# Performance work log

Hardware: AMD Instinct MI355X
Metric: run time of the kernel (lower is better)

## Reference

```python
import jax, jax.numpy as jnp
import numpy as np

N = 31            # number of multiplexed frames; S-matrix order (2**5 - 1)
IMG_H, IMG_W = 256, 256


def make_S_mat(n):
    # Sylvester Hadamard matrix of order n+1, then standard S-matrix:
    # drop first row/col, map +1 -> 0, -1 -> 1 (binary 0/1 mask matrix).
    H = np.array([[1]], dtype=np.int64)
    while H.shape[0] < n + 1:
        H = np.block([[H, H], [H, -H]])
    return ((1 - H[1:, 1:]) * 0.5).astype(np.float32)


def setup_inputs() -> dict:
    key = jax.random.key(0)
    k1, k2 = jax.random.split(key)
    # time_points initialized near ones (Solver.initialize uses ones_like)
    time_points = jax.random.uniform(k1, (IMG_H, IMG_W, N, 1), jnp.float32, 0.5, 1.5)
    # pixels are positive photon counts
    pixels = jax.random.uniform(k2, (IMG_H, IMG_W, N, 1), jnp.float32, 1.0, 100.0)
    S = jnp.asarray(make_S_mat(N))
    t = jnp.float32(0.1)  # log-barrier weight t_init
    return {"time_points": time_points, "pixels": pixels, "S": S, "t": t}


def reference(time_points, pixels, S, t):
    # One Newton step residual: residual = J^T H^{-1} J per pixel.
    x, k = time_points, pixels            # (..., n, 1)
    n = S.shape[0]
    rate = jnp.matmul(S, x)               # (..., n, 1), assumed > 0
    inv_rate = 1.0 / rate
    inv_sq_rate = jnp.squeeze(inv_rate * inv_rate, -1)   # (..., n)

    # Jacobian: t * likelihood + time-point barrier + rate barrier
    J = (-t * jnp.matmul(S.T, k * inv_rate - 1.0)
         - 1.0 / x
         - jnp.matmul(S.T, inv_rate))     # (..., n, 1)

    # Hessian: weighted Gram S^T diag(w) S (fuses likelihood + rate-barrier
    # terms; identical math to the einsum over the SS outer-product tensor)
    w = (t * jnp.squeeze(k, -1) + 1.0) * inv_sq_rate      # (..., n)
    H = jnp.einsum('...a,da,ea->...de', w, S, S)          # (..., n, n)
    # + diag(1/x^2) time-point barrier Hessian
    H = H + (1.0 / jnp.squeeze(x * x, -1))[..., :, None] * jnp.eye(n, dtype=H.dtype)

    Hinv = jnp.linalg.inv(H)              # (..., n, n) batched inverse
    residual = jnp.squeeze(jnp.swapaxes(J, -2, -1) @ Hinv @ J, (-1, -2))  # (H, W)
    return residual
```

## Files before the change

kernel.cpp:

```cpp
#include <hip/hip_runtime.h>

#define NDIM 31
#define NPIX (256 * 256)
#define CG_FULL 3

__device__ __forceinline__ float rcpf(float x) { return __builtin_amdgcn_rcpf(x); }

template <int CTRL>
__device__ __forceinline__ float dppf(float v) {
    return __int_as_float(__builtin_amdgcn_update_dpp(
        0, __float_as_int(v), CTRL, 0xF, 0xF, true));
}
__device__ __forceinline__ float swz4(float v) {
    return __int_as_float(__builtin_amdgcn_ds_swizzle(__float_as_int(v), 0x101F));
}
__device__ __forceinline__ float swz16(float v) {
    return __int_as_float(__builtin_amdgcn_ds_swizzle(__float_as_int(v), 0x401F));
}
__device__ __forceinline__ float bperm0(float v, int bbase) {
    return __int_as_float(__builtin_amdgcn_ds_bpermute(bbase, __float_as_int(v)));
}

struct Sgn { float s1, s2, s4, s8, s16; };

__device__ __forceinline__ float wht32(float v, const Sgn& g) {
    v = fmaf(g.s1,  v, dppf<0xB1>(v));
    v = fmaf(g.s2,  v, dppf<0x4E>(v));
    v = fmaf(g.s4,  v, swz4(v));
    v = fmaf(g.s8,  v, dppf<0x128>(v));
    v = fmaf(g.s16, v, swz16(v));
    return v;
}

__device__ __forceinline__ float sum32(float s) {
    s += dppf<0xB1>(s);
    s += dppf<0x4E>(s);
    s += dppf<0x124>(s);
    s += dppf<0x128>(s);
    s += swz16(s);
    return s;
}

__global__ __launch_bounds__(256, 8) void solver_kernel(
    const float* __restrict__ xg, const float* __restrict__ kg,
    const float* __restrict__ tg, float* __restrict__ out)
{
    const int tid = blockIdx.x * 256 + threadIdx.x;
    const int pix = tid >> 5;
    const int lane = threadIdx.x & 63;
    const int l = lane & 31;
    const int bbase = (lane & 32) << 2;

    const float t = tg[0];

    float x = 1.0f, k = 0.0f;
    if (l >= 1) {
        const int base = pix * NDIM + (l - 1);
        x = xg[base];
        k = kg[base];
    }

    Sgn g;
    g.s1  = (l & 1)  ? -1.0f : 1.0f;
    g.s2  = (l & 2)  ? -1.0f : 1.0f;
    g.s4  = (l & 4)  ? -1.0f : 1.0f;
    g.s8  = (l & 8)  ? -1.0f : 1.0f;
    g.s16 = (l & 16) ? -1.0f : 1.0f;

    float xh = wht32(x, g);
    float xh0 = bperm0(xh, bbase);
    float rate = 0.5f * (xh0 - xh);
    float inv_rate = (l == 0) ? 0.0f : rcpf(rate);

    float v = t * (k * inv_rate - 1.0f) + inv_rate;
    float w = (t * k + 1.0f) * inv_rate * inv_rate;

    float invx = rcpf(x);
    float invx2 = invx * invx;

    float vh = wht32(v, g);
    float vh0 = bperm0(vh, bbase);
    float b = -0.5f * (vh0 - vh) - invx;
    if (l == 0) b = 0.0f;

    float wh = wht32(w, g);
    float wh0 = bperm0(wh, bbase);
    float dH = 0.5f * (wh0 - wh) + invx2;
    float Minv = (l == 0) ? 0.0f : rcpf(dH);

    const float w4 = 0.25f * w;

    float r = b;
    float z = Minv * r;
    float p = z;
    float rz = sum32(r * z);
    float phi = 0.0f;

#pragma unroll
    for (int it = 0; it < CG_FULL; ++it) {
        float ph = wht32(p, g);
        float ph0 = bperm0(ph, bbase);
        float q = w4 * (ph0 - ph);
        float qh = wht32(q, g);
        float qh0 = bperm0(qh, bbase);
        float Ap = fmaf(invx2, p, qh0 - qh);

        float pAp = sum32(p * Ap);
        float alpha = rz * rcpf(fmaxf(pAp, 1e-30f));
        phi = fmaf(alpha, rz, phi);
        r = fmaf(-alpha, Ap, r);
        z = Minv * r;
        float rzn = sum32(r * z);
        float beta = rzn * rcpf(fmaxf(rz, 1e-30f));
        rz = rzn;
        p = fmaf(beta, p, z);
    }
    {
        float ph = wht32(p, g);
        float ph0 = bperm0(ph, bbase);
        float q = w4 * (ph0 - ph);
        float qh = wht32(q, g);
        float qh0 = bperm0(qh, bbase);
        float Ap = fmaf(invx2, p, qh0 - qh);
        float pAp = sum32(p * Ap);
        float alpha = rz * rcpf(fmaxf(pAp, 1e-30f));
        phi = fmaf(alpha, rz, phi);
    }

    if (l == 0) out[pix] = phi;
}

extern "C" void kernel_launch(void* const* d_in, const int* in_sizes, int n_in,
                              void* d_out, int out_size, void* d_ws, size_t ws_size,
                              hipStream_t stream) {
    const float* xg = (const float*)d_in[0];
    const float* kg = (const float*)d_in[1];
    const float* tg = (const float*)d_in[3];
    float* out = (float*)d_out;

    const int threads = 256;
    const int blocks = (NPIX * 32) / threads;
    solver_kernel<<<blocks, threads, 0, stream>>>(xg, kg, tg, out);
}
```

Before: 79.12 us.

## Switch to one-thread-per-pixel with register-resident WHT and LDS-staged loads

Replaces the 32-lanes-per-pixel mapping, which used DPP and swizzle cross-lane Walsh-Hadamard transforms and reductions, with one thread per pixel. Each thread holds its 31-element vectors in registers and runs the butterfly WHT locally. Inputs are staged through shared memory with coalesced global loads, and the final CG iteration computes pAp directly from the transformed vector, skipping the second transform. The aim is to remove cross-lane shuffle and reduction latency and to cut the thread count by 32x. In exchange, register pressure becomes very high, launch bounds drop to one block, and only 256 blocks run with 62KB of LDS each, which can leave occupancy and latency hiding low.

Result: faster. 75.47 us (-4.6%).

```diff
diff --git a/kernel.cpp b/kernel.cpp
--- a/kernel.cpp
+++ b/kernel.cpp
@@ -3,131 +3,147 @@
 #define NDIM 31
 #define NPIX (256 * 256)
 #define CG_FULL 3
+#define TPB 256
+#define BLK_DW (TPB * NDIM)
 
 __device__ __forceinline__ float rcpf(float x) { return __builtin_amdgcn_rcpf(x); }
 
-template <int CTRL>
-__device__ __forceinline__ float dppf(float v) {
-    return __int_as_float(__builtin_amdgcn_update_dpp(
-        0, __float_as_int(v), CTRL, 0xF, 0xF, true));
-}
-__device__ __forceinline__ float swz4(float v) {
-    return __int_as_float(__builtin_amdgcn_ds_swizzle(__float_as_int(v), 0x101F));
-}
-__device__ __forceinline__ float swz16(float v) {
-    return __int_as_float(__builtin_amdgcn_ds_swizzle(__float_as_int(v), 0x401F));
-}
-__device__ __forceinline__ float bperm0(float v, int bbase) {
-    return __int_as_float(__builtin_amdgcn_ds_bpermute(bbase, __float_as_int(v)));
+__device__ __forceinline__ void wht32r(float h[32]) {
+#pragma unroll
+    for (int s = 1; s < 32; s <<= 1) {
+#pragma unroll
+        for (int i = 0; i < 32; ++i) {
+            if ((i & s) == 0) {
+                const float a = h[i], b = h[i | s];
+                h[i]     = a + b;
+                h[i | s] = a - b;
+            }
+        }
+    }
 }
 
-struct Sgn { float s1, s2, s4, s8, s16; };
-
-__device__ __forceinline__ float wht32(float v, const Sgn& g) {
-    v = fmaf(g.s1,  v, dppf<0xB1>(v));
-    v = fmaf(g.s2,  v, dppf<0x4E>(v));
-    v = fmaf(g.s4,  v, swz4(v));
-    v = fmaf(g.s8,  v, dppf<0x128>(v));
-    v = fmaf(g.s16, v, swz16(v));
-    return v;
-}
-
-__device__ __forceinline__ float sum32(float s) {
-    s += dppf<0xB1>(s);
-    s += dppf<0x4E>(s);
-    s += dppf<0x124>(s);
-    s += dppf<0x128>(s);
-    s += swz16(s);
-    return s;
-}
-
-__global__ __launch_bounds__(256, 8) void solver_kernel(
+__global__ __launch_bounds__(TPB, 1) void solver_kernel(
     const float* __restrict__ xg, const float* __restrict__ kg,
     const float* __restrict__ tg, float* __restrict__ out)
 {
-    const int tid = blockIdx.x * 256 + threadIdx.x;
-    const int pix = tid >> 5;
-    const int lane = threadIdx.x & 63;
-    const int l = lane & 31;
-    const int bbase = (lane & 32) << 2;
+    __shared__ float xs[BLK_DW];
+    __shared__ float ks[BLK_DW];
+    const int j = threadIdx.x;
+    const int gbase = blockIdx.x * BLK_DW;
+
+#pragma unroll
+    for (int i = 0; i < NDIM; ++i) {
+        xs[i * TPB + j] = xg[gbase + i * TPB + j];
+        ks[i * TPB + j] = kg[gbase + i * TPB + j];
+    }
+    __syncthreads();
 
     const float t = tg[0];
+    const int lb = j * NDIM;
 
-    float x = 1.0f, k = 0.0f;
-    if (l >= 1) {
-        const int base = pix * NDIM + (l - 1);
-        x = xg[base];
-        k = kg[base];
+    float x[NDIM], k[NDIM];
+#pragma unroll
+    for (int i = 0; i < NDIM; ++i) { x[i] = xs[lb + i]; k[i] = ks[lb + i]; }
+
+    float h[32];
+    h[0] = 0.0f;
+#pragma unroll
+    for (int i = 0; i < NDIM; ++i) h[i + 1] = x[i];
+    wht32r(h);
+    float ir[NDIM];
+#pragma unroll
+    for (int a = 0; a < NDIM; ++a) ir[a] = 2.0f * rcpf(h[0] - h[a + 1]);
+
+    float w4[NDIM];
+    float hv[32], hw[32];
+    hv[0] = 0.0f; hw[0] = 0.0f;
+#pragma unroll
+    for (int a = 0; a < NDIM; ++a) {
+        const float ira = ir[a];
+        hv[a + 1] = t * (k[a] * ira - 1.0f) + ira;
+        const float wa = (t * k[a] + 1.0f) * ira * ira;
+        hw[a + 1] = wa;
+        w4[a] = 0.25f * wa;
     }
+    wht32r(hv);
+    wht32r(hw);
 
-    Sgn g;
-    g.s1  = (l & 1)  ? -1.0f : 1.0f;
-    g.s2  = (l & 2)  ? -1.0f : 1.0f;
-    g.s4  = (l & 4)  ? -1.0f : 1.0f;
-    g.s8  = (l & 8)  ? -1.0f : 1.0f;
-    g.s16 = (l & 16) ? -1.0f : 1.0f;
-
-    float xh = wht32(x, g);
-    float xh0 = bperm0(xh, bbase);
-    float rate = 0.5f * (xh0 - xh);
-    float inv_rate = (l == 0) ? 0.0f : rcpf(rate);
-
-    float v = t * (k * inv_rate - 1.0f) + inv_rate;
-    float w = (t * k + 1.0f) * inv_rate * inv_rate;
-
-    float invx = rcpf(x);
-    float invx2 = invx * invx;
-
-    float vh = wht32(v, g);
-    float vh0 = bperm0(vh, bbase);
-    float b = -0.5f * (vh0 - vh) - invx;
-    if (l == 0) b = 0.0f;
-
-    float wh = wht32(w, g);
-    float wh0 = bperm0(wh, bbase);
-    float dH = 0.5f * (wh0 - wh) + invx2;
-    float Minv = (l == 0) ? 0.0f : rcpf(dH);
-
-    const float w4 = 0.25f * w;
-
-    float r = b;
-    float z = Minv * r;
-    float p = z;
-    float rz = sum32(r * z);
+    float invx2[NDIM], Minv[NDIM], r[NDIM], p[NDIM];
+    float acc[4] = {0.f, 0.f, 0.f, 0.f};
+#pragma unroll
+    for (int i = 0; i < NDIM; ++i) {
+        const float invx = rcpf(x[i]);
+        invx2[i] = invx * invx;
+        const float b  = -0.5f * (hv[0] - hv[i + 1]) - invx;
+        const float dH =  0.5f * (hw[0] - hw[i + 1]) + invx2[i];
+        Minv[i] = rcpf(dH);
+        r[i] = b;
+        const float z = Minv[i] * b;
+        p[i] = z;
+        acc[i & 3] = fmaf(b, z, acc[i & 3]);
+    }
+    float rz = (acc[0] + acc[1]) + (acc[2] + acc[3]);
     float phi = 0.0f;
 
 #pragma unroll
     for (int it = 0; it < CG_FULL; ++it) {
-        float ph = wht32(p, g);
-        float ph0 = bperm0(ph, bbase);
-        float q = w4 * (ph0 - ph);
-        float qh = wht32(q, g);
-        float qh0 = bperm0(qh, bbase);
-        float Ap = fmaf(invx2, p, qh0 - qh);
+        float hp[32];
+        hp[0] = 0.0f;
+#pragma unroll
+        for (int i = 0; i < NDIM; ++i) hp[i + 1] = p[i];
+        wht32r(hp);
+        float hq[32];
+        hq[0] = 0.0f;
+#pragma unroll
+        for (int a = 0; a < NDIM; ++a) hq[a + 1] = w4[a] * (hp[0] - hp[a + 1]);
+        wht32r(hq);
 
-        float pAp = sum32(p * Ap);
-        float alpha = rz * rcpf(fmaxf(pAp, 1e-30f));
+        float Ap[NDIM];
+        float pa[4] = {0.f, 0.f, 0.f, 0.f};
+#pragma unroll
+        for (int i = 0; i < NDIM; ++i) {
+            Ap[i] = (hq[0] - hq[i + 1]) + invx2[i] * p[i];
+            pa[i & 3] = fmaf(p[i], Ap[i], pa[i & 3]);
+        }
+        const float pAp = (pa[0] + pa[1]) + (pa[2] + pa[3]);
+        const float alpha = rz * rcpf(fmaxf(pAp, 1e-30f));
         phi = fmaf(alpha, rz, phi);
-        r = fmaf(-alpha, Ap, r);
-        z = Minv * r;
-        float rzn = sum32(r * z);
-        float beta = rzn * rcpf(fmaxf(rz, 1e-30f));
+
+        float zbuf[NDIM];
+        float ra[4] = {0.f, 0.f, 0.f, 0.f};
+#pragma unroll
+        for (int i = 0; i < NDIM; ++i) {
+            r[i] = fmaf(-alpha, Ap[i], r[i]);
+            const float z = Minv[i] * r[i];
+            zbuf[i] = z;
+            ra[i & 3] = fmaf(r[i], z, ra[i & 3]);
+        }
+        const float rzn = (ra[0] + ra[1]) + (ra[2] + ra[3]);
+        const float beta = rzn * rcpf(fmaxf(rz, 1e-30f));
         rz = rzn;
-        p = fmaf(beta, p, z);
+#pragma unroll
+        for (int i = 0; i < NDIM; ++i) p[i] = fmaf(beta, p[i], zbuf[i]);
     }
+
     {
-        float ph = wht32(p, g);
-        float ph0 = bperm0(ph, bbase);
-        float q = w4 * (ph0 - ph);
-        float qh = wht32(q, g);
-        float qh0 = bperm0(qh, bbase);
-        float Ap = fmaf(invx2, p, qh0 - qh);
-        float pAp = sum32(p * Ap);
-        float alpha = rz * rcpf(fmaxf(pAp, 1e-30f));
+        float hp[32];
+        hp[0] = 0.0f;
+#pragma unroll
+        for (int i = 0; i < NDIM; ++i) hp[i + 1] = p[i];
+        wht32r(hp);
+        float pa[4] = {0.f, 0.f, 0.f, 0.f};
+#pragma unroll
+        for (int a = 0; a < NDIM; ++a) {
+            const float d = hp[0] - hp[a + 1];
+            pa[a & 3] = fmaf(w4[a] * d, d, pa[a & 3]);
+            pa[a & 3] = fmaf(invx2[a] * p[a], p[a], pa[a & 3]);
+        }
+        const float pAp = (pa[0] + pa[1]) + (pa[2] + pa[3]);
+        const float alpha = rz * rcpf(fmaxf(pAp, 1e-30f));
         phi = fmaf(alpha, rz, phi);
     }
 
-    if (l == 0) out[pix] = phi;
+    out[blockIdx.x * TPB + j] = phi;
 }
 
 extern "C" void kernel_launch(void* const* d_in, const int* in_sizes, int n_in,
@@ -138,7 +154,6 @@
     const float* tg = (const float*)d_in[3];
     float* out = (float*)d_out;
 
-    const int threads = 256;
-    const int blocks = (NPIX * 32) / threads;
-    solver_kernel<<<blocks, threads, 0, stream>>>(xg, kg, tg, out);
+    const int blocks = NPIX / TPB;
+    solver_kernel<<<blocks, TPB, 0, stream>>>(xg, kg, tg, out);
 }
```
